# Performance work log

Measured on AMD Instinct MI355X. Metric: run time of the kernel, lower is better.

The kernel has to match this reference:

```python
import jax, jax.numpy as jnp
import numpy as np


def setup_inputs() -> dict:
    key = jax.random.key(0)
    k1, k2, k3, k4 = jax.random.split(key, 4)
    n_nodes, n_edges, d_in, d_half = 100000, 1600000, 256, 128
    x = jax.random.normal(k1, (n_nodes, d_in), dtype=jnp.float32)
    edge_index = jax.random.randint(k2, (2, n_edges), 0, n_nodes, dtype=jnp.int64)
    W_f = jax.random.normal(k3, (d_half, d_in), dtype=jnp.float32) * (1.0 / np.sqrt(d_in))
    W_b = jax.random.normal(k4, (d_half, d_in), dtype=jnp.float32) * (1.0 / np.sqrt(d_in))
    bias_param = jnp.zeros((2 * d_half,), dtype=jnp.float32)
    return {"x": x, "edge_index": edge_index, "W_f": W_f, "W_b": W_b, "bias_param": bias_param}


def _inv_sqrt(deg):
    # deg.pow(-0.5) with inf -> 0
    return jnp.where(deg > 0, jax.lax.rsqrt(deg), 0.0)


def reference(x, edge_index, W_f, W_b, bias_param):
    n_nodes = x.shape[0]
    # add_remaining_self_loops with fill value 1
    loops = jnp.arange(n_nodes, dtype=edge_index.dtype)
    ei = jnp.concatenate([edge_index, jnp.stack([loops, loops])], axis=1)
    n_e = ei.shape[1]
    w = jnp.ones((n_e,), dtype=x.dtype)
    # directed_norm, flow='source_to_target': col, row = edge_index
    col, row = ei[0], ei[1]
    in_deg = jax.ops.segment_sum(w, col, num_segments=n_nodes)
    out_deg = jax.ops.segment_sum(w, row, num_segments=n_nodes)
    ew = _inv_sqrt(out_deg)[row] * w * _inv_sqrt(in_deg)[col]  # [E]
    # adj_forward: source=row, target=col ; adj_backward: source=col, target=row
    mf = (x @ W_f.T)[row] * ew[:, None]           # [E, d_half]
    y_forward = jax.ops.segment_sum(mf, col, num_segments=n_nodes)
    mb = (x @ W_b.T)[col] * ew[:, None]           # [E, d_half]
    y_backward = jax.ops.segment_sum(mb, row, num_segments=n_nodes)
    y = jnp.concatenate([y_forward, y_backward], axis=-1) + bias_param
    return y
```

## Files before the change

### kernel.cpp

```cpp
#include <hip/hip_runtime.h>

#define D_IN 256
#define D_HALF 128

typedef __attribute__((ext_vector_type(8))) short short8;
typedef __attribute__((ext_vector_type(4))) float float4v;

__device__ __forceinline__ unsigned short f2bf(float f) {
    union { float f; unsigned u; } v; v.f = f;
    unsigned r = v.u + 0x7FFF + ((v.u >> 16) & 1);
    return (unsigned short)(r >> 16);
}
__device__ __forceinline__ float bflo(unsigned u) { union { unsigned u; float f; } v; v.u = u << 16; return v.f; }
__device__ __forceinline__ float bfhi(unsigned u) { union { unsigned u; float f; } v; v.u = u & 0xffff0000u; return v.f; }

__device__ __forceinline__ void async16(const void* g, void* l) {
    __builtin_amdgcn_global_load_lds(
        (const __attribute__((address_space(1))) unsigned int*)g,
        (__attribute__((address_space(3))) unsigned int*)l, 16, 0, 0);
}


#define S_SH 9
#define NBK_MAX 512
#define CAP 12288
#define EPB 4096

__global__ void zero_kernel(int* __restrict__ gcnt) {
    int i = blockIdx.x * blockDim.x + threadIdx.x;
    if (i < NBK_MAX) gcnt[i] = 0;
}

__global__ void p1_cast_kernel(const int* __restrict__ col, const int* __restrict__ row,
                               int* __restrict__ gcnt, unsigned* __restrict__ staging,
                               int N, int E, int nP1,
                               const float* __restrict__ x, const float* __restrict__ Wf,
                               const float* __restrict__ Wb, unsigned short* __restrict__ xb,
                               unsigned short* __restrict__ wcat, int n4) {
    __shared__ int hist[NBK_MAX];
    __shared__ int base_[NBK_MAX];
    const int tid = threadIdx.x;

    if (blockIdx.x >= nP1) {
        int i = (blockIdx.x - nP1) * 256 + tid;
        const int w4 = (2 * D_HALF * D_IN) / 4;
        if (i < n4) {
            float4 v = ((const float4*)x)[i];
            ushort4 o = { f2bf(v.x), f2bf(v.y), f2bf(v.z), f2bf(v.w) };
            ((ushort4*)xb)[i] = o;
        } else if (i < n4 + w4) {
            int j = i - n4;
            int elem = j * 4;
            const float* src = (elem < D_HALF * D_IN) ? (Wf + elem) : (Wb + (elem - D_HALF * D_IN));
            float4 v = *(const float4*)src;
            ushort4 o = { f2bf(v.x), f2bf(v.y), f2bf(v.z), f2bf(v.w) };
            ((ushort4*)wcat)[j] = o;
        }
        return;
    }

    hist[tid] = 0; hist[tid + 256] = 0;
    __syncthreads();

    int ce[16], re[16], rf_[16], rb_[16];
    const int e0 = blockIdx.x * EPB;
    #pragma unroll
    for (int j = 0; j < 16; ++j) {
        int e = e0 + j * 256 + tid;
        if (e < E) {
            ce[j] = col[e];
            re[j] = row[e];
            rf_[j] = atomicAdd(&hist[ce[j] >> S_SH], 1);
            rb_[j] = atomicAdd(&hist[(N + re[j]) >> S_SH], 1);
        } else {
            ce[j] = -1; re[j] = 0; rf_[j] = 0; rb_[j] = 0;
        }
    }
    __syncthreads();

    #pragma unroll
    for (int b = 0; b < NBK_MAX / 256; ++b) {
        int idx = b * 256 + tid;
        int c = hist[idx];
        if (c) base_[idx] = idx * CAP + atomicAdd(&gcnt[idx], c);
    }
    __syncthreads();

    #pragma unroll
    for (int j = 0; j < 16; ++j) {
        if (ce[j] >= 0) {
            int c = ce[j], r = re[j];
            staging[(size_t)base_[c >> S_SH] + rf_[j]] =
                ((unsigned)(c & 511) << 23) | (unsigned)r;
            int sb = N + r;
            staging[(size_t)base_[sb >> S_SH] + rb_[j]] =
                ((unsigned)(sb & 511) << 23) | (unsigned)c;
        }
    }
}

__global__ void bsort_kernel(const unsigned* __restrict__ staging, const int* __restrict__ gcnt,
                             int* __restrict__ cnt, int* __restrict__ offs,
                             float* __restrict__ inv_in, float* __restrict__ inv_out,
                             int* __restrict__ adj, int N, int M) {
    __shared__ int lcnt[NBK_MAX];
    __shared__ int s[256];
    __shared__ int lbuf[CAP];
    __shared__ int bc[2];
    const int tid = threadIdx.x;
    const int b = blockIdx.x;
    const int s0 = b << S_SH;

    int g0 = gcnt[2 * tid], g1 = gcnt[2 * tid + 1];
    int pairB = g0 + g1;
    s[tid] = pairB;
    __syncthreads();
    for (int d = 1; d < 256; d <<= 1) {
        int t = (tid >= d) ? s[tid - d] : 0;
        __syncthreads();
        s[tid] += t;
        __syncthreads();
    }
    if (tid == (b >> 1)) {
        int excl = s[tid] - pairB;
        bc[0] = excl + ((b & 1) ? g0 : 0);
        bc[1] = (b & 1) ? g1 : g0;
    }
    lcnt[tid] = 0; lcnt[tid + 256] = 0;
    __syncthreads();

    const int base = bc[0];
    const int count = bc[1];
    const unsigned* __restrict__ st = staging + (size_t)b * CAP;

    for (int i = tid; i < count; i += 256)
        atomicAdd(&lcnt[st[i] >> 23], 1);
    __syncthreads();

    int v0 = lcnt[2 * tid], v1 = lcnt[2 * tid + 1];
    int pair = v0 + v1;
    s[tid] = pair;
    __syncthreads();
    for (int d = 1; d < 256; d <<= 1) {
        int t = (tid >= d) ? s[tid - d] : 0;
        __syncthreads();
        s[tid] += t;
        __syncthreads();
    }
    int excl = s[tid] - pair;

    int gs0 = s0 + 2 * tid;
    if (gs0 < M) {
        cnt[gs0] = v0;  offs[gs0] = base + excl;
        if (gs0 < N) inv_in[gs0] = rsqrtf((float)(v0 + 1));
        else         inv_out[gs0 - N] = rsqrtf((float)(v0 + 1));
    }
    if (gs0 + 1 < M) {
        cnt[gs0 + 1] = v1;  offs[gs0 + 1] = base + excl + v0;
        if (gs0 + 1 < N) inv_in[gs0 + 1] = rsqrtf((float)(v1 + 1));
        else             inv_out[gs0 + 1 - N] = rsqrtf((float)(v1 + 1));
    }

    lcnt[2 * tid] = excl;
    lcnt[2 * tid + 1] = excl + v0;
    __syncthreads();

    for (int i = tid; i < count; i += 256) {
        unsigned it = st[i];
        int sl = it >> 23;
        int p = atomicAdd(&lcnt[sl], 1);
        lbuf[p] = (int)(it & 0x7fffffu);
    }
    __syncthreads();
    for (int i = tid; i < count; i += 256)
        adj[base + i] = lbuf[i];
}


#define BM 128
#define BN 128
#define BK 32

__global__ void gemm_mfma_kernel(const unsigned short* __restrict__ xb,
                                 const unsigned short* __restrict__ wcat,
                                 const float* __restrict__ inv_in,
                                 const float* __restrict__ inv_out,
                                 unsigned short* __restrict__ zb, int N) {
    __shared__ __align__(16) unsigned short As[BM * BK];
    __shared__ __align__(16) unsigned short Bs[BN * BK];
    const int tid = threadIdx.x;
    const int wave = tid >> 6;
    const int lane = tid & 63;
    const int bm = blockIdx.x * BM;
    const int bn = blockIdx.y * BN;
    const int warpM = wave >> 1;
    const int warpN = wave & 1;
    const int l15 = lane & 15;
    const int quad = lane >> 4;

    float4v acc[4][4];
    #pragma unroll
    for (int i = 0; i < 4; ++i)
        #pragma unroll
        for (int j = 0; j < 4; ++j)
            acc[i][j] = (float4v){0.f, 0.f, 0.f, 0.f};

    for (int kt = 0; kt < D_IN / BK; ++kt) {
        #pragma unroll
        for (int iss = 0; iss < 2; ++iss) {
            const int pbase = iss * 256 + wave * 64;
            const int p = pbase + lane;
            const int m = p >> 2;
            const int g = (p & 3) ^ ((m >> 1) & 3);
            int gm = bm + m; if (gm >= N) gm = N - 1;
            async16(xb + (size_t)gm * D_IN + kt * BK + g * 8, &As[pbase * 8]);
            async16(wcat + (size_t)(bn + m) * D_IN + kt * BK + g * 8, &Bs[pbase * 8]);
        }
        __syncthreads();

        short8 af[4], bfr[4];
        #pragma unroll
        for (int mi = 0; mi < 4; ++mi) {
            int m = warpM * 64 + mi * 16 + l15;
            af[mi] = *(const short8*)&As[m * BK + (quad ^ ((m >> 1) & 3)) * 8];
        }
        #pragma unroll
        for (int ni = 0; ni < 4; ++ni) {
            int n = warpN * 64 + ni * 16 + l15;
            bfr[ni] = *(const short8*)&Bs[n * BK + (quad ^ ((n >> 1) & 3)) * 8];
        }
        #pragma unroll
        for (int mi = 0; mi < 4; ++mi)
            #pragma unroll
            for (int ni = 0; ni < 4; ++ni)
                acc[mi][ni] = __builtin_amdgcn_mfma_f32_16x16x32_bf16(af[mi], bfr[ni], acc[mi][ni], 0, 0, 0);
        __syncthreads();
    }

    const float* __restrict__ sc = (blockIdx.y == 0) ? inv_out : inv_in;
    #pragma unroll
    for (int mi = 0; mi < 4; ++mi) {
        #pragma unroll
        for (int reg = 0; reg < 4; ++reg) {
            int gm = bm + warpM * 64 + mi * 16 + quad * 4 + reg;
            if (gm < N) {
                float s = sc[gm];
                #pragma unroll
                for (int ni = 0; ni < 4; ++ni) {
                    int gn = bn + warpN * 64 + ni * 16 + l15;
                    zb[(size_t)gm * D_IN + gn] = f2bf(acc[mi][ni][reg] * s);
                }
            }
        }
    }
}


__global__ void gather_kernel(const unsigned short* __restrict__ zb, const int* __restrict__ adj,
                              const int* __restrict__ offs, const int* __restrict__ cnt,
                              const float* __restrict__ inv_in, const float* __restrict__ inv_out,
                              const float* __restrict__ bias,
                              float* __restrict__ out, int N) {
    const int wave = threadIdx.x >> 6;
    const int lane = threadIdx.x & 63;
    const int slot = blockIdx.x * 4 + wave;
    if (slot >= 2 * N) return;
    const int dir = (slot >= N) ? 1 : 0;
    const int node = slot - dir * N;
    const int csr = slot;
    const int beg = offs[csr];
    const int deg = cnt[csr];
    const int end = beg + deg;
    const int g4 = lane >> 4;
    const int l15 = lane & 15;
    const int chu = dir * D_HALF + 8 * l15;
    const int pa = g4 << 2;

    float a0 = 0.f, a1 = 0.f, a2 = 0.f, a3 = 0.f;
    float a4 = 0.f, a5 = 0.f, a6 = 0.f, a7 = 0.f;

    for (int base = beg; base < end; base += 64) {
        int len = end - base; if (len > 64) len = 64;
        int nb = (lane < len) ? adj[base + lane] : node;
        #pragma unroll 8
        for (int j0 = 0; j0 < len; j0 += 4) {
            int nsel = __builtin_amdgcn_ds_bpermute((j0 << 2) + pa, nb);
            float m = (j0 + g4 < len) ? 1.0f : 0.0f;
            const uint4 u = *(const uint4*)&zb[(size_t)nsel * D_IN + chu];
            a0 = fmaf(m, bflo(u.x), a0); a1 = fmaf(m, bfhi(u.x), a1);
            a2 = fmaf(m, bflo(u.y), a2); a3 = fmaf(m, bfhi(u.y), a3);
            a4 = fmaf(m, bflo(u.z), a4); a5 = fmaf(m, bfhi(u.z), a5);
            a6 = fmaf(m, bflo(u.w), a6); a7 = fmaf(m, bfhi(u.w), a7);
        }
    }

    a0 += __shfl_xor(a0, 16); a0 += __shfl_xor(a0, 32);
    a1 += __shfl_xor(a1, 16); a1 += __shfl_xor(a1, 32);
    a2 += __shfl_xor(a2, 16); a2 += __shfl_xor(a2, 32);
    a3 += __shfl_xor(a3, 16); a3 += __shfl_xor(a3, 32);
    a4 += __shfl_xor(a4, 16); a4 += __shfl_xor(a4, 32);
    a5 += __shfl_xor(a5, 16); a5 += __shfl_xor(a5, 32);
    a6 += __shfl_xor(a6, 16); a6 += __shfl_xor(a6, 32);
    a7 += __shfl_xor(a7, 16); a7 += __shfl_xor(a7, 32);

    if (g4 == 0) {
        const uint4 us = *(const uint4*)&zb[(size_t)node * D_IN + chu];
        a0 += bflo(us.x); a1 += bfhi(us.x);
        a2 += bflo(us.y); a3 += bfhi(us.y);
        a4 += bflo(us.z); a5 += bfhi(us.z);
        a6 += bflo(us.w); a7 += bfhi(us.w);

        const float scale = dir ? inv_out[node] : inv_in[node];
        const float4 bv0 = *(const float4*)&bias[chu];
        const float4 bv1 = *(const float4*)&bias[chu + 4];
        size_t oi = (size_t)node * D_IN + chu;
        float4 o0 = { bv0.x + scale * a0, bv0.y + scale * a1,
                      bv0.z + scale * a2, bv0.w + scale * a3 };
        float4 o1 = { bv1.x + scale * a4, bv1.y + scale * a5,
                      bv1.z + scale * a6, bv1.w + scale * a7 };
        *(float4*)&out[oi] = o0;
        *(float4*)&out[oi + 4] = o1;
    }
}


extern "C" void kernel_launch(void* const* d_in, const int* in_sizes, int n_in,
                              void* d_out, int out_size, void* d_ws, size_t ws_size,
                              hipStream_t stream) {
    const float* x    = (const float*)d_in[0];
    const int*   ei   = (const int*)d_in[1];
    const float* Wf   = (const float*)d_in[2];
    const float* Wb   = (const float*)d_in[3];
    const float* bias = (const float*)d_in[4];
    float* out = (float*)d_out;

    const int N = in_sizes[0] / D_IN;
    const int E = in_sizes[1] / 2;
    const int* col = ei;
    const int* rowp = ei + E;

    char* ws = (char*)d_ws;
    unsigned short* xb = (unsigned short*)ws;   ws += (size_t)N * D_IN * sizeof(short);
    unsigned short* zb = (unsigned short*)ws;   ws += (size_t)N * D_IN * sizeof(short);
    unsigned short* wcat = (unsigned short*)ws; ws += (size_t)2 * D_HALF * D_IN * sizeof(short);
    int* cnt = (int*)ws;            ws += (size_t)2 * N * sizeof(int);
    int* offs = (int*)ws;           ws += (size_t)2 * N * sizeof(int);
    float* inv_in = (float*)ws;     ws += (size_t)N * sizeof(float);
    float* inv_out = (float*)ws;    ws += (size_t)N * sizeof(float);
    int* adj = (int*)ws;            ws += (size_t)2 * E * sizeof(int);
    int* gcnt = (int*)ws;           ws += NBK_MAX * sizeof(int);

    unsigned* staging = (unsigned*)zb;

    const int M = 2 * N;
    const int nbuck = (M + 511) >> S_SH;
    const int nP1 = (E + EPB - 1) / EPB;
    const int n4 = N * D_IN / 4;
    const int w4 = (2 * D_HALF * D_IN) / 4;
    const int nCast = (n4 + w4 + 255) / 256;

    zero_kernel<<<2, 256, 0, stream>>>(gcnt);
    p1_cast_kernel<<<nP1 + nCast, 256, 0, stream>>>(col, rowp, gcnt, staging, N, E, nP1,
                                                    x, Wf, Wb, xb, wcat, n4);
    bsort_kernel<<<nbuck, 256, 0, stream>>>(staging, gcnt, cnt, offs, inv_in, inv_out, adj, N, M);

    dim3 ggrid((N + BM - 1) / BM, D_IN / BN);
    gemm_mfma_kernel<<<ggrid, 256, 0, stream>>>(xb, wcat, inv_in, inv_out, zb, N);

    gather_kernel<<<(2 * N + 3) / 4, 256, 0, stream>>>(zb, adj, offs, cnt, inv_in, inv_out, bias, out, N);
}
```

Measured before the change: 380.6 us.

## Widen GEMM tile to full output width and move preprocessing to 512-thread blocks

The GEMM now has each block compute the full 256-column output (forward and backward halves) for its 128 rows, so the x tile is loaded once instead of twice. Each wave holds twice as many accumulators, and launch bounds allow only one block per SM, which cuts occupancy. The bucketing and sort kernels move to 512-thread blocks, with one histogram bucket per thread and fewer edges per block, so the loops and scans are simpler. The cost is more register pressure and fewer resident waves in the GEMM.

```diff
diff --git a/kernel.cpp b/kernel.cpp
--- a/kernel.cpp
+++ b/kernel.cpp
@@ -24,25 +24,26 @@
 #define S_SH 9
 #define NBK_MAX 512
 #define CAP 12288
-#define EPB 4096
+#define EPB 2048
 
 __global__ void zero_kernel(int* __restrict__ gcnt) {
     int i = blockIdx.x * blockDim.x + threadIdx.x;
     if (i < NBK_MAX) gcnt[i] = 0;
 }
 
-__global__ void p1_cast_kernel(const int* __restrict__ col, const int* __restrict__ row,
-                               int* __restrict__ gcnt, unsigned* __restrict__ staging,
-                               int N, int E, int nP1,
-                               const float* __restrict__ x, const float* __restrict__ Wf,
-                               const float* __restrict__ Wb, unsigned short* __restrict__ xb,
-                               unsigned short* __restrict__ wcat, int n4) {
+__global__ __launch_bounds__(512)
+void p1_cast_kernel(const int* __restrict__ col, const int* __restrict__ row,
+                    int* __restrict__ gcnt, unsigned* __restrict__ staging,
+                    int N, int E, int nP1,
+                    const float* __restrict__ x, const float* __restrict__ Wf,
+                    const float* __restrict__ Wb, unsigned short* __restrict__ xb,
+                    unsigned short* __restrict__ wcat, int n4) {
     __shared__ int hist[NBK_MAX];
     __shared__ int base_[NBK_MAX];
     const int tid = threadIdx.x;
 
     if (blockIdx.x >= nP1) {
-        int i = (blockIdx.x - nP1) * 256 + tid;
+        int i = (blockIdx.x - nP1) * 512 + tid;
         const int w4 = (2 * D_HALF * D_IN) / 4;
         if (i < n4) {
             float4 v = ((const float4*)x)[i];
@@ -59,14 +60,14 @@
         return;
     }
 
-    hist[tid] = 0; hist[tid + 256] = 0;
-    __syncthreads();
-
-    int ce[16], re[16], rf_[16], rb_[16];
+    hist[tid] = 0;
+    __syncthreads();
+
+    int ce[4], re[4], rf_[4], rb_[4];
     const int e0 = blockIdx.x * EPB;
     #pragma unroll
-    for (int j = 0; j < 16; ++j) {
-        int e = e0 + j * 256 + tid;
+    for (int j = 0; j < 4; ++j) {
+        int e = e0 + j * 512 + tid;
         if (e < E) {
             ce[j] = col[e];
             re[j] = row[e];
@@ -78,16 +79,14 @@
     }
     __syncthreads();
 
+    {
+        int c = hist[tid];
+        if (c) base_[tid] = tid * CAP + atomicAdd(&gcnt[tid], c);
+    }
+    __syncthreads();
+
     #pragma unroll
-    for (int b = 0; b < NBK_MAX / 256; ++b) {
-        int idx = b * 256 + tid;
-        int c = hist[idx];
-        if (c) base_[idx] = idx * CAP + atomicAdd(&gcnt[idx], c);
-    }
-    __syncthreads();
-
-    #pragma unroll
-    for (int j = 0; j < 16; ++j) {
+    for (int j = 0; j < 4; ++j) {
         if (ce[j] >= 0) {
             int c = ce[j], r = re[j];
             staging[(size_t)base_[c >> S_SH] + rf_[j]] =
@@ -99,110 +98,99 @@
     }
 }
 
-__global__ void bsort_kernel(const unsigned* __restrict__ staging, const int* __restrict__ gcnt,
-                             int* __restrict__ cnt, int* __restrict__ offs,
-                             float* __restrict__ inv_in, float* __restrict__ inv_out,
-                             int* __restrict__ adj, int N, int M) {
+__global__ __launch_bounds__(512)
+void bsort_kernel(const unsigned* __restrict__ staging, const int* __restrict__ gcnt,
+                  int* __restrict__ cnt, int* __restrict__ offs,
+                  float* __restrict__ inv_in, float* __restrict__ inv_out,
+                  int* __restrict__ adj, int N, int M) {
     __shared__ int lcnt[NBK_MAX];
-    __shared__ int s[256];
+    __shared__ int s[NBK_MAX];
     __shared__ int lbuf[CAP];
     __shared__ int bc[2];
     const int tid = threadIdx.x;
     const int b = blockIdx.x;
     const int s0 = b << S_SH;
 
-    int g0 = gcnt[2 * tid], g1 = gcnt[2 * tid + 1];
-    int pairB = g0 + g1;
-    s[tid] = pairB;
-    __syncthreads();
-    for (int d = 1; d < 256; d <<= 1) {
+    int g = gcnt[tid];
+    s[tid] = g;
+    __syncthreads();
+    for (int d = 1; d < 512; d <<= 1) {
         int t = (tid >= d) ? s[tid - d] : 0;
         __syncthreads();
         s[tid] += t;
         __syncthreads();
     }
-    if (tid == (b >> 1)) {
-        int excl = s[tid] - pairB;
-        bc[0] = excl + ((b & 1) ? g0 : 0);
-        bc[1] = (b & 1) ? g1 : g0;
-    }
-    lcnt[tid] = 0; lcnt[tid + 256] = 0;
+    if (tid == b) { bc[0] = s[tid] - g; bc[1] = g; }
+    lcnt[tid] = 0;
     __syncthreads();
 
     const int base = bc[0];
     const int count = bc[1];
     const unsigned* __restrict__ st = staging + (size_t)b * CAP;
 
-    for (int i = tid; i < count; i += 256)
+    for (int i = tid; i < count; i += 512)
         atomicAdd(&lcnt[st[i] >> 23], 1);
     __syncthreads();
 
-    int v0 = lcnt[2 * tid], v1 = lcnt[2 * tid + 1];
-    int pair = v0 + v1;
-    s[tid] = pair;
-    __syncthreads();
-    for (int d = 1; d < 256; d <<= 1) {
+    int v = lcnt[tid];
+    s[tid] = v;
+    __syncthreads();
+    for (int d = 1; d < 512; d <<= 1) {
         int t = (tid >= d) ? s[tid - d] : 0;
         __syncthreads();
         s[tid] += t;
         __syncthreads();
     }
-    int excl = s[tid] - pair;
-
-    int gs0 = s0 + 2 * tid;
-    if (gs0 < M) {
-        cnt[gs0] = v0;  offs[gs0] = base + excl;
-        if (gs0 < N) inv_in[gs0] = rsqrtf((float)(v0 + 1));
-        else         inv_out[gs0 - N] = rsqrtf((float)(v0 + 1));
-    }
-    if (gs0 + 1 < M) {
-        cnt[gs0 + 1] = v1;  offs[gs0 + 1] = base + excl + v0;
-        if (gs0 + 1 < N) inv_in[gs0 + 1] = rsqrtf((float)(v1 + 1));
-        else             inv_out[gs0 + 1 - N] = rsqrtf((float)(v1 + 1));
-    }
-
-    lcnt[2 * tid] = excl;
-    lcnt[2 * tid + 1] = excl + v0;
-    __syncthreads();
-
-    for (int i = tid; i < count; i += 256) {
+    int excl = s[tid] - v;
+
+    int gs = s0 + tid;
+    if (gs < M) {
+        cnt[gs] = v;  offs[gs] = base + excl;
+        float iv = rsqrtf((float)(v + 1));
+        if (gs < N) inv_in[gs] = iv;
+        else        inv_out[gs - N] = iv;
+    }
+
+    lcnt[tid] = excl;
+    __syncthreads();
+
+    for (int i = tid; i < count; i += 512) {
         unsigned it = st[i];
         int sl = it >> 23;
         int p = atomicAdd(&lcnt[sl], 1);
         lbuf[p] = (int)(it & 0x7fffffu);
     }
     __syncthreads();
-    for (int i = tid; i < count; i += 256)
+    for (int i = tid; i < count; i += 512)
         adj[base + i] = lbuf[i];
 }
 
 
 #define BM 128
-#define BN 128
 #define BK 32
 
-__global__ void gemm_mfma_kernel(const unsigned short* __restrict__ xb,
-                                 const unsigned short* __restrict__ wcat,
-                                 const float* __restrict__ inv_in,
-                                 const float* __restrict__ inv_out,
-                                 unsigned short* __restrict__ zb, int N) {
+__global__ __launch_bounds__(256, 1)
+void gemm_mfma_kernel(const unsigned short* __restrict__ xb,
+                      const unsigned short* __restrict__ wcat,
+                      const float* __restrict__ inv_in,
+                      const float* __restrict__ inv_out,
+                      unsigned short* __restrict__ zb, int N) {
     __shared__ __align__(16) unsigned short As[BM * BK];
-    __shared__ __align__(16) unsigned short Bs[BN * BK];
+    __shared__ __align__(16) unsigned short Bs[256 * BK];
     const int tid = threadIdx.x;
     const int wave = tid >> 6;
     const int lane = tid & 63;
     const int bm = blockIdx.x * BM;
-    const int bn = blockIdx.y * BN;
     const int warpM = wave >> 1;
     const int warpN = wave & 1;
     const int l15 = lane & 15;
     const int quad = lane >> 4;
 
-    float4v acc[4][4];
+    float4v acc[4][8];
     #pragma unroll
     for (int i = 0; i < 4; ++i)
         #pragma unroll
-        for (int j = 0; j < 4; ++j)
+        for (int j = 0; j < 8; ++j)
             acc[i][j] = (float4v){0.f, 0.f, 0.f, 0.f};
 
     for (int kt = 0; kt < D_IN / BK; ++kt) {
@@ -214,30 +202,37 @@
             const int g = (p & 3) ^ ((m >> 1) & 3);
             int gm = bm + m; if (gm >= N) gm = N - 1;
             async16(xb + (size_t)gm * D_IN + kt * BK + g * 8, &As[pbase * 8]);
-            async16(wcat + (size_t)(bn + m) * D_IN + kt * BK + g * 8, &Bs[pbase * 8]);
-        }
-        __syncthreads();
-
-        short8 af[4], bfr[4];
+        }
+        #pragma unroll
+        for (int iss = 0; iss < 4; ++iss) {
+            const int pbase = iss * 256 + wave * 64;
+            const int p = pbase + lane;
+            const int m = p >> 2;
+            const int g = (p & 3) ^ ((m >> 1) & 3);
+            async16(wcat + (size_t)m * D_IN + kt * BK + g * 8, &Bs[pbase * 8]);
+        }
+        __syncthreads();
+
+        short8 af[4], bfr[8];
         #pragma unroll
         for (int mi = 0; mi < 4; ++mi) {
             int m = warpM * 64 + mi * 16 + l15;
             af[mi] = *(const short8*)&As[m * BK + (quad ^ ((m >> 1) & 3)) * 8];
         }
         #pragma unroll
-        for (int ni = 0; ni < 4; ++ni) {
-            int n = warpN * 64 + ni * 16 + l15;
+        for (int ni = 0; ni < 8; ++ni) {
+            int n = warpN * 128 + ni * 16 + l15;
             bfr[ni] = *(const short8*)&Bs[n * BK + (quad ^ ((n >> 1) & 3)) * 8];
         }
         #pragma unroll
         for (int mi = 0; mi < 4; ++mi)
             #pragma unroll
-            for (int ni = 0; ni < 4; ++ni)
+            for (int ni = 0; ni < 8; ++ni)
                 acc[mi][ni] = __builtin_amdgcn_mfma_f32_16x16x32_bf16(af[mi], bfr[ni], acc[mi][ni], 0, 0, 0);
         __syncthreads();
     }
 
-    const float* __restrict__ sc = (blockIdx.y == 0) ? inv_out : inv_in;
+    const float* __restrict__ sc = (warpN == 0) ? inv_out : inv_in;
     #pragma unroll
     for (int mi = 0; mi < 4; ++mi) {
         #pragma unroll
@@ -246,8 +241,8 @@
             if (gm < N) {
                 float s = sc[gm];
                 #pragma unroll
-                for (int ni = 0; ni < 4; ++ni) {
-                    int gn = bn + warpN * 64 + ni * 16 + l15;
+                for (int ni = 0; ni < 8; ++ni) {
+                    int gn = warpN * 128 + ni * 16 + l15;
                     zb[(size_t)gm * D_IN + gn] = f2bf(acc[mi][ni][reg] * s);
                 }
             }
@@ -357,15 +352,14 @@
     const int nP1 = (E + EPB - 1) / EPB;
     const int n4 = N * D_IN / 4;
     const int w4 = (2 * D_HALF * D_IN) / 4;
-    const int nCast = (n4 + w4 + 255) / 256;
+    const int nCast = (n4 + w4 + 511) / 512;
 
     zero_kernel<<<2, 256, 0, stream>>>(gcnt);
-    p1_cast_kernel<<<nP1 + nCast, 256, 0, stream>>>(col, rowp, gcnt, staging, N, E, nP1,
+    p1_cast_kernel<<<nP1 + nCast, 512, 0, stream>>>(col, rowp, gcnt, staging, N, E, nP1,
                                                     x, Wf, Wb, xb, wcat, n4);
-    bsort_kernel<<<nbuck, 256, 0, stream>>>(staging, gcnt, cnt, offs, inv_in, inv_out, adj, N, M);
-
-    dim3 ggrid((N + BM - 1) / BM, D_IN / BN);
-    gemm_mfma_kernel<<<ggrid, 256, 0, stream>>>(xb, wcat, inv_in, inv_out, zb, N);
+    bsort_kernel<<<nbuck, 512, 0, stream>>>(staging, gcnt, cnt, offs, inv_in, inv_out, adj, N, M);
+
+    gemm_mfma_kernel<<<(N + BM - 1) / BM, 256, 0, stream>>>(xb, wcat, inv_in, inv_out, zb, N);
 
     gather_kernel<<<(2 * N + 3) / 4, 256, 0, stream>>>(zb, adj, offs, cnt, inv_in, inv_out, bias, out, N);
 }
```

After: 408.1 us. +7.2%, slower.

## Stage bucket scatter in LDS for coalesced writes, split gather by direction

Applied to the files above, without the earlier changes.

The partition kernel now sorts each block's edge records by bucket in shared memory, using a prefix scan over the local histogram. It then writes them to the global staging buffer as contiguous runs instead of scattered 4-byte stores, which is meant to cut uncoalesced global write traffic. This adds about 48KB of LDS per block, which may lower occupancy for the cast blocks sharing the kernel. The zero kernel is replaced with a memset, and the gather is split into two launches, one per direction, likely to improve cache locality of the zb half being read.

```diff
diff --git a/kernel.cpp b/kernel.cpp
--- a/kernel.cpp
+++ b/kernel.cpp
@@ -25,11 +25,6 @@
 #define NBK_MAX 512
 #define CAP 12288
 #define EPB 4096
-
-__global__ void zero_kernel(int* __restrict__ gcnt) {
-    int i = blockIdx.x * blockDim.x + threadIdx.x;
-    if (i < NBK_MAX) gcnt[i] = 0;
-}
 
 __global__ void p1_cast_kernel(const int* __restrict__ col, const int* __restrict__ row,
                                int* __restrict__ gcnt, unsigned* __restrict__ staging,
@@ -39,6 +34,10 @@
                                unsigned short* __restrict__ wcat, int n4) {
     __shared__ int hist[NBK_MAX];
     __shared__ int base_[NBK_MAX];
+    __shared__ int lstart[NBK_MAX];
+    __shared__ int s[256];
+    __shared__ unsigned lbuf[2 * EPB];
+    __shared__ unsigned short lbk[2 * EPB];
     const int tid = threadIdx.x;
 
     if (blockIdx.x >= nP1) {
@@ -78,24 +77,44 @@
     }
     __syncthreads();
 
-    #pragma unroll
-    for (int b = 0; b < NBK_MAX / 256; ++b) {
-        int idx = b * 256 + tid;
-        int c = hist[idx];
-        if (c) base_[idx] = idx * CAP + atomicAdd(&gcnt[idx], c);
-    }
-    __syncthreads();
+    int c0 = hist[2 * tid], c1 = hist[2 * tid + 1];
+    if (c0) base_[2 * tid]     = (2 * tid) * CAP     + atomicAdd(&gcnt[2 * tid], c0);
+    if (c1) base_[2 * tid + 1] = (2 * tid + 1) * CAP + atomicAdd(&gcnt[2 * tid + 1], c1);
+    int pair = c0 + c1;
+    s[tid] = pair;
+    __syncthreads();
+    for (int d = 1; d < 256; d <<= 1) {
+        int t = (tid >= d) ? s[tid - d] : 0;
+        __syncthreads();
+        s[tid] += t;
+        __syncthreads();
+    }
+    int excl = s[tid] - pair;
+    lstart[2 * tid] = excl;
+    lstart[2 * tid + 1] = excl + c0;
+    __syncthreads();
+    const int total = s[255];
 
     #pragma unroll
     for (int j = 0; j < 16; ++j) {
         if (ce[j] >= 0) {
             int c = ce[j], r = re[j];
-            staging[(size_t)base_[c >> S_SH] + rf_[j]] =
-                ((unsigned)(c & 511) << 23) | (unsigned)r;
+            int bf = c >> S_SH;
+            int pf = lstart[bf] + rf_[j];
+            lbuf[pf] = ((unsigned)(c & 511) << 23) | (unsigned)r;
+            lbk[pf] = (unsigned short)bf;
             int sb = N + r;
-            staging[(size_t)base_[sb >> S_SH] + rb_[j]] =
-                ((unsigned)(sb & 511) << 23) | (unsigned)c;
-        }
+            int bb = sb >> S_SH;
+            int pb = lstart[bb] + rb_[j];
+            lbuf[pb] = ((unsigned)(sb & 511) << 23) | (unsigned)c;
+            lbk[pb] = (unsigned short)bb;
+        }
+    }
+    __syncthreads();
+
+    for (int i = tid; i < total; i += 256) {
+        int bk = lbk[i];
+        staging[(size_t)base_[bk] + (i - lstart[bk])] = lbuf[i];
     }
 }
 
@@ -260,16 +279,16 @@
                               const int* __restrict__ offs, const int* __restrict__ cnt,
                               const float* __restrict__ inv_in, const float* __restrict__ inv_out,
                               const float* __restrict__ bias,
-                              float* __restrict__ out, int N) {
+                              float* __restrict__ out, int N, int slotBase, int nSlots) {
     const int wave = threadIdx.x >> 6;
     const int lane = threadIdx.x & 63;
-    const int slot = blockIdx.x * 4 + wave;
-    if (slot >= 2 * N) return;
+    const int li = blockIdx.x * 4 + wave;
+    if (li >= nSlots) return;
+    const int slot = slotBase + li;
     const int dir = (slot >= N) ? 1 : 0;
     const int node = slot - dir * N;
-    const int csr = slot;
-    const int beg = offs[csr];
-    const int deg = cnt[csr];
+    const int beg = offs[slot];
+    const int deg = cnt[slot];
     const int end = beg + deg;
     const int g4 = lane >> 4;
     const int l15 = lane & 15;
@@ -359,13 +378,13 @@
     const int w4 = (2 * D_HALF * D_IN) / 4;
     const int nCast = (n4 + w4 + 255) / 256;
 
-    zero_kernel<<<2, 256, 0, stream>>>(gcnt);
+    hipMemsetAsync(gcnt, 0, NBK_MAX * sizeof(int), stream);
     p1_cast_kernel<<<nP1 + nCast, 256, 0, stream>>>(col, rowp, gcnt, staging, N, E, nP1,
                                                     x, Wf, Wb, xb, wcat, n4);
     bsort_kernel<<<nbuck, 256, 0, stream>>>(staging, gcnt, cnt, offs, inv_in, inv_out, adj, N, M);
 
-    dim3 ggrid((N + BM - 1) / BM, D_IN / BN);
-    gemm_mfma_kernel<<<ggrid, 256, 0, stream>>>(xb, wcat, inv_in, inv_out, zb, N);
-
-    gather_kernel<<<(2 * N + 3) / 4, 256, 0, stream>>>(zb, adj, offs, cnt, inv_in, inv_out, bias, out, N);
-}
+    gemm_mfma_kernel<<<dim3((N + BM - 1) / BM, D_IN / BN), 256, 0, stream>>>(xb, wcat, inv_in, inv_out, zb, N);
+
+    gather_kernel<<<(N + 3) / 4, 256, 0, stream>>>(zb, adj, offs, cnt, inv_in, inv_out, bias, out, N, 0, N);
+    gather_kernel<<<(N + 3) / 4, 256, 0, stream>>>(zb, adj, offs, cnt, inv_in, inv_out, bias, out, N, N, N);
+}
```

Result: slower. 404.6 us (+6.3%).
